# Optimization experiments

Measured on AMD Instinct MI355X. Metric: run time of the kernel, lower is better.

## Reference

```python
import jax, jax.numpy as jnp
import numpy as np


def setup_inputs() -> dict:
    N, E, F, M, D = 50000, 200000, 64, 64, 128
    L = 3
    LAMBS = jnp.array([1.0, 0.1, 0.01], jnp.float32) * 12.0  # lambs * output
    R = int(np.ceil(np.sqrt(N)))  # n_virtuals = 224
    RAW = M * L + F  # raw_message_dimension = 256
    key = jax.random.key(0)
    ks = jax.random.split(key, 16)

    def lin(k, i, o):
        return jax.random.normal(k, (i, o), jnp.float32) / np.float32(np.sqrt(i))

    return dict(
        source_nodes=jax.random.randint(ks[0], (E,), 0, N),
        target_nodes=jax.random.randint(ks[1], (E,), 0, N),
        timestamps=jax.random.uniform(ks[2], (E,), jnp.float32),
        now_time=jnp.ones((1,), jnp.float32),
        predict_IND=0,
        node_features=0.1 * jax.random.normal(ks[3], (N, F), jnp.float32),
        memory=jnp.concatenate([0.05 * jax.random.normal(ks[4], (N, L, M), jnp.float32), jnp.ones((N, L, 1), jnp.float32)], axis=-1),
        last_update=jnp.zeros((N,), jnp.float32),
        virtual_memory=0.05 * jax.random.normal(ks[5], (R, L, M), jnp.float32),
        virtual_last_update=jnp.zeros((R,), jnp.float32),
        A_r=jnp.ones((N, R), jnp.float32) + jax.random.uniform(ks[6], (N, R), jnp.float32) / 10.0,
        static_emb=0.1 * jax.random.normal(ks[7], (N, D), jnp.float32),
        lamb=jnp.array([0.5], jnp.float32),
        lambs=LAMBS,
        mf_W1=lin(ks[8], RAW, RAW // 2), mf_b1=jnp.zeros((RAW // 2,), jnp.float32),
        mf_W2=lin(ks[9], RAW // 2, M), mf_b2=jnp.zeros((M,), jnp.float32),
        ffr_W1=lin(ks[10], RAW, RAW), ffr_b1=jnp.zeros((RAW,), jnp.float32),
        ffr_W2=lin(ks[11], RAW, M), ffr_b2=jnp.zeros((M,), jnp.float32),
        et_W=lin(ks[12], L * M, M), et_b=jnp.zeros((M,), jnp.float32),
        st_W=lin(ks[13], 2 * M, D), st_b=jnp.zeros((D,), jnp.float32),
    )


def reference(source_nodes, target_nodes, timestamps, now_time, predict_IND,
              node_features, memory, last_update, virtual_memory, virtual_last_update,
              A_r, static_emb, lamb, lambs,
              mf_W1, mf_b1, mf_W2, mf_b2, ffr_W1, ffr_b1, ffr_W2, ffr_b2,
              et_W, et_b, st_W, st_b):
    N, L, Mp1 = memory.shape
    M = Mp1 - 1
    R = virtual_memory.shape[0]
    E = source_nodes.shape[0]
    eps = 1e-6

    # exp_lambs embedding of targets: memory ratio [E, L*M]
    mem_t = memory[target_nodes]
    tgt_emb = (mem_t[:, :, :-1] / mem_t[:, :, -1:]).reshape(E, L * M)
    # raw message = [target_embedding, node_features[target], 1]  -> [E, RAW+1]
    src_msg = jnp.concatenate([tgt_emb, node_features[target_nodes], jnp.ones((E, 1), tgt_emb.dtype)], axis=1)

    # exp_lambs aggregation: decay every event to the latest timestamp of its source node
    t_max = jax.ops.segment_max(timestamps, source_nodes, num_segments=N)
    cnt = jax.ops.segment_sum(jnp.ones((E,), timestamps.dtype), source_nodes, num_segments=N)
    has_msg = cnt > 0
    t_max = jnp.where(has_msg, t_max, 0.0)
    w = jnp.exp(-lambs[None, :] * (t_max[source_nodes][:, None] - timestamps[:, None]))  # [E, L]
    agg = jax.ops.segment_sum(w[:, :, None] * src_msg[:, None, :], source_nodes, num_segments=N)  # [N, L, RAW+1]

    # MLP message function on feature channels, carry the weight-count channel along
    feat = agg[:, :, :-1]  # [N, L, RAW]
    h = jax.nn.relu(feat @ mf_W1 + mf_b1)
    msg_feat = jax.nn.relu(h @ mf_W2 + mf_b2)  # [N, L, M]
    messages = jnp.concatenate([msg_feat, agg[:, :, -1:]], axis=-1)  # [N, L, M+1]

    # virtual-node routing: A = softmax(A_r, axis=0) restricted to active nodes
    A = jax.nn.softmax(A_r, axis=0) * has_msg[:, None].astype(A_r.dtype)  # [N, R]
    B = jnp.where(has_msg[:, None, None], feat / jnp.maximum(agg[:, :, -1:], eps), 0.0)  # [N, L, RAW]
    vmid = jnp.einsum('nr,nlf->rlf', A, B)  # [R, L, RAW]
    vh = jax.nn.leaky_relu(vmid @ ffr_W1 + ffr_b1)
    vmsg = jax.nn.leaky_relu(vh @ ffr_W2 + ffr_b2)  # [R, L, M]

    # node memory exp-decay update (only active nodes)
    dt = jnp.where(has_msg, t_max - last_update, 0.0)
    decay = jnp.exp(-lambs[None, :, None] * dt[:, None, None])  # [N, L, 1]
    new_mem = jnp.where(has_msg[:, None, None], memory * decay + messages, memory)
    node_emb = (new_mem[:, :, :-1] / jnp.maximum(new_mem[:, :, -1:], eps)).reshape(N, L * M)

    # virtual memory exp-decay update to now_time
    vdt = now_time[0] - virtual_last_update  # [R]
    vdecay = jnp.exp(-lambs[None, :] * vdt[:, None])  # [R, L]
    new_vmem = virtual_memory * vdecay[:, :, None] + vmsg
    v_emb = new_vmem.reshape(R, L * M)

    r2n = jax.nn.softmax(A_r, axis=1)  # [N, R]
    vnode_emb = r2n @ v_emb  # [N, L*M]

    dyn = jnp.concatenate([node_emb, vnode_emb], axis=0)  # [2N, L*M]
    hh = jax.nn.leaky_relu(dyn @ et_W + et_b)  # [2N, M]
    hh = hh.reshape(2, N, M).transpose(1, 0, 2).reshape(N, 2 * M)
    spat = jax.nn.leaky_relu(hh @ st_W + st_b)  # [N, D]
    return lamb[0] * static_emb + (1.0 - lamb[0]) * spat
```

## Files before the change

kernel.cpp:

```cpp
#include <hip/hip_runtime.h>

static __device__ __forceinline__ float lky(float x) { return x > 0.f ? x : 0.01f * x; }

static __device__ __forceinline__ unsigned short f2bf(float x) {
    unsigned int u = __float_as_uint(x);
    unsigned int r = (u + 0x7FFFu + ((u >> 16) & 1u)) >> 16;
    return (unsigned short)r;
}
static __device__ __forceinline__ float bf2f(unsigned short x) {
    return __uint_as_float((unsigned int)x << 16);
}
static __device__ __forceinline__ unsigned int pack2bf(float lo, float hi) {
    return (unsigned int)f2bf(lo) | ((unsigned int)f2bf(hi) << 16);
}

typedef __attribute__((ext_vector_type(8))) short short8;
typedef __attribute__((ext_vector_type(4))) float f32x4;

constexpr int SN  = 50048;
constexpr int KLV = 608;
constexpr int VCM = 83;
constexpr int NSCAN = 53248;
constexpr int NWG_V = 12 * VCM;
constexpr int NQ_V  = NWG_V / 8;
constexpr int NR_V  = NWG_V % 8;
constexpr int AGG_BLOCKS = 2048;
constexpr int AGG_WAVES  = AGG_BLOCKS * 4;
constexpr int SETUP_BLOCKS = 2048;
constexpr int SETUP_WAVES  = SETUP_BLOCKS * 4;

__global__ __launch_bounds__(256) void k_setup(
        float* t_max, int* cnt, int* cursor, float* colsum,
        const float* __restrict__ mf_W1, unsigned short* __restrict__ W1T,
        const float* __restrict__ mf_W2, unsigned short* __restrict__ W2T,
        const float* __restrict__ et_W,  unsigned short* __restrict__ etWT,
        const float* __restrict__ st_W,  unsigned short* __restrict__ stWT,
        const float* __restrict__ memory, const float* __restrict__ nodef,
        unsigned int* __restrict__ temb, int N, int NP) {
    int gid = blockIdx.x * 256 + threadIdx.x;
    if (gid < N) { t_max[gid] = -1.0f; cursor[gid] = 0; }
    if (gid < NP) cnt[gid] = 0;
    if (gid < 224) colsum[gid] = 0.0f;
    if (gid < 128 * 256) {
        int c = gid / 256, k = gid % 256;
        W1T[gid] = f2bf(mf_W1[k * 128 + c]);
    } else if (gid < 128 * 256 + 64 * 128) {
        int i = gid - 128 * 256;
        int c = i / 128, k = i % 128;
        W2T[i] = f2bf(mf_W2[k * 64 + c]);
    } else if (gid < 128 * 256 + 64 * 128 + 64 * 192) {
        int i = gid - (128 * 256 + 64 * 128);
        int c = i / 192, k = i % 192;
        etWT[i] = f2bf(et_W[k * 64 + c]);
    } else if (gid < 128 * 256 + 64 * 128 + 64 * 192 + 128 * 128) {
        int i = gid - (128 * 256 + 64 * 128 + 64 * 192);
        int c = i / 128, k = i % 128;
        stWT[i] = f2bf(st_W[k * 128 + c]);
    }
    int gw = blockIdx.x * 4 + (threadIdx.x >> 6);
    int lane = threadIdx.x & 63;
    for (int n = gw; n < N; n += SETUP_WAVES) {
        const float* mrow = memory + (size_t)n * 195;
        float d0 = mrow[64], d1 = mrow[129], d2 = mrow[194];
        int f = 2 * lane;
        float den = (f < 64) ? d0 : d1;
        int offA = (f < 64) ? f : f + 1;
        float va0 = mrow[offA] / den;
        float va1 = mrow[offA + 1] / den;
        float vb0, vb1;
        if (lane < 32) {
            vb0 = mrow[130 + 2 * lane] / d2;
            vb1 = mrow[131 + 2 * lane] / d2;
        } else {
            const float* nf = nodef + (size_t)n * 64 + 2 * (lane - 32);
            vb0 = nf[0]; vb1 = nf[1];
        }
        temb[(size_t)n * 128 + lane]      = pack2bf(va0, va1);
        temb[(size_t)n * 128 + 64 + lane] = pack2bf(vb0, vb1);
    }
}

__global__ void k_tmax_cnt(const int* __restrict__ src, const float* __restrict__ ts,
                           float* t_max, int* cnt, int E) {
    int e = blockIdx.x * 256 + threadIdx.x;
    if (e >= E) return;
    int s = src[e];
    atomicMax((int*)(t_max + s), __float_as_int(ts[e]));
    atomicAdd(cnt + s, 1);
}

__global__ __launch_bounds__(1024) void k_scan(const int* __restrict__ cnt,
                                               int* __restrict__ offsets, int N) {
    __shared__ int wsum[16];
    __shared__ int s_run;
    int t = threadIdx.x;
    int lane = t & 63, wid = t >> 6;
    if (t == 0) s_run = 0;
    __syncthreads();
    int nchunk = (N + 4095) >> 12;
    for (int c = 0; c < nchunk; ++c) {
        int i0 = (c << 12) + t * 4;
        int4 v = *(const int4*)(cnt + i0);
        int s = v.x + v.y + v.z + v.w;
        int x = s;
        #pragma unroll
        for (int d = 1; d < 64; d <<= 1) {
            int y = __shfl_up(x, d, 64);
            if (lane >= d) x += y;
        }
        if (lane == 63) wsum[wid] = x;
        __syncthreads();
        int wbase = 0;
        #pragma unroll
        for (int w = 0; w < 16; ++w) wbase += (w < wid) ? wsum[w] : 0;
        int run = s_run;
        int base = run + wbase + x - s;
        if (i0 + 3 < N) {
            int4 o;
            o.x = base; o.y = base + v.x; o.z = o.y + v.y; o.w = o.z + v.z;
            *(int4*)(offsets + i0) = o;
        } else {
            int o = base;
            if (i0 < N) offsets[i0] = o;
            o += v.x;
            if (i0 + 1 < N) offsets[i0 + 1] = o;
            o += v.y;
            if (i0 + 2 < N) offsets[i0 + 2] = o;
            o += v.z;
            if (i0 + 3 < N) offsets[i0 + 3] = o;
        }
        __syncthreads();
        if (t == 1023) s_run = run + wbase + x;
        __syncthreads();
    }
    if (t == 0) offsets[N] = s_run;
}

__global__ void k_scatter(const int* __restrict__ src, const int* __restrict__ tgt,
                          const float* __restrict__ ts, const int* __restrict__ offsets,
                          int* cursor, int2* __restrict__ edat, int E) {
    int e = blockIdx.x * 256 + threadIdx.x;
    if (e >= E) return;
    int s = src[e];
    int pos = offsets[s] + atomicAdd(cursor + s, 1);
    edat[pos] = make_int2(tgt[e], __float_as_int(ts[e]));
}

__global__ __launch_bounds__(256) void k_aexp(
        const float* __restrict__ A_r,
        float* __restrict__ rowsum, float* __restrict__ colsum,
        unsigned short* __restrict__ AexpT, unsigned short* __restrict__ Aexp_rm, int N) {
    __shared__ unsigned short sE[64][228];
    int t = threadIdx.x;
    int n0 = blockIdx.x * 64;
    int maxq = min(64, N - n0) * 56;
    const float4* src = (const float4*)(A_r + (size_t)n0 * 224);
    #pragma unroll
    for (int k = 0; k < 14; ++k) {
        int i = t + k * 256;
        float4 v = (i < maxq) ? src[i] : (float4){-1e30f, -1e30f, -1e30f, -1e30f};
        int row = i / 56, cq = i % 56;
        uint2 pk;
        pk.x = pack2bf(__expf(v.x), __expf(v.y));
        pk.y = pack2bf(__expf(v.z), __expf(v.w));
        *(uint2*)&sE[row][cq * 4] = pk;
    }
    __syncthreads();
    {
        int row = t >> 2, q = t & 3;
        const uint2* p = (const uint2*)&sE[row][q * 56];
        float s = 0.f;
        #pragma unroll
        for (int c = 0; c < 7; ++c) {
            uint2 u = p[c];
            s += __uint_as_float(u.x << 16) + __uint_as_float(u.x & 0xffff0000u)
               + __uint_as_float(u.y << 16) + __uint_as_float(u.y & 0xffff0000u);
        }
        s += __shfl_xor(s, 1, 64);
        s += __shfl_xor(s, 2, 64);
        if (q == 0 && n0 + row < N) rowsum[n0 + row] = s;
    }
    if (t < 224) {
        float s = 0.f;
        #pragma unroll 8
        for (int r = 0; r < 64; ++r) s += bf2f(sE[r][t]);
        atomicAdd(colsum + t, s);
    }
    {
        unsigned int* dst = (unsigned int*)Aexp_rm;
        for (int i = t; i < 64 * 112; i += 256) {
            int n = i / 112, cp = i % 112;
            dst[(size_t)(n0 + n) * 112 + cp] = *(const unsigned int*)&sE[n][2 * cp];
        }
    }
    {
        unsigned int* dst = (unsigned int*)AexpT;
        for (int u = t; u < 224 * 32; u += 256) {
            int r = u >> 5, np = u & 31;
            unsigned int lo = sE[2 * np][r];
            unsigned int hi = sE[2 * np + 1][r];
            dst[(size_t)r * (SN / 2) + (n0 >> 1) + np] = lo | (hi << 16);
        }
    }
}

__global__ __launch_bounds__(256) void k_agg(
        const int2* __restrict__ edat, const int* __restrict__ offsets,
        const float* __restrict__ t_max, const unsigned int* __restrict__ temb,
        const float* __restrict__ lambs,
        unsigned int* __restrict__ aggb, float* __restrict__ cnt3,
        int* __restrict__ has_msg, int N) {
    int gw = blockIdx.x * 4 + (threadIdx.x >> 6);
    int lane = threadIdx.x & 63;
    float lb0 = lambs[0], lb1 = lambs[1], lb2 = lambs[2];
    for (int n = gw; n < SN; n += AGG_WAVES) {
        size_t rb = (size_t)n * 3;
        if (n >= N) {
            #pragma unroll
            for (int l = 0; l < 3; ++l) {
                unsigned int* row = aggb + (rb + l) * 128;
                row[lane] = 0; row[64 + lane] = 0;
                if (lane == 0) cnt3[rb + l] = 0.f;
            }
            continue;
        }
        int beg = offsets[n], end = offsets[n + 1];
        float tm = t_max[n];
        float aa0[3], aa1[3], ab0[3], ab1[3], accc[3];
        #pragma unroll
        for (int l = 0; l < 3; ++l) { aa0[l] = aa1[l] = ab0[l] = ab1[l] = accc[l] = 0.f; }
        for (int idx = beg; idx < end; ++idx) {
            int2 ed = edat[idx];
            int tt = ed.x;
            float d = tm - __int_as_float(ed.y);
            unsigned int ua = temb[(size_t)tt * 128 + lane];
            unsigned int ub = temb[(size_t)tt * 128 + 64 + lane];
            float a0 = __uint_as_float(ua << 16);
            float a1 = __uint_as_float(ua & 0xffff0000u);
            float b0 = __uint_as_float(ub << 16);
            float b1 = __uint_as_float(ub & 0xffff0000u);
            float w0 = __expf(-lb0 * d), w1 = __expf(-lb1 * d), w2 = __expf(-lb2 * d);
            aa0[0] += w0 * a0; aa1[0] += w0 * a1; ab0[0] += w0 * b0; ab1[0] += w0 * b1; accc[0] += w0;
            aa0[1] += w1 * a0; aa1[1] += w1 * a1; ab0[1] += w1 * b0; ab1[1] += w1 * b1; accc[1] += w1;
            aa0[2] += w2 * a0; aa1[2] += w2 * a1; ab0[2] += w2 * b0; ab1[2] += w2 * b1; accc[2] += w2;
        }
        #pragma unroll
        for (int l = 0; l < 3; ++l) {
            unsigned int* row = aggb + (rb + l) * 128;
            row[lane]      = pack2bf(aa0[l], aa1[l]);
            row[64 + lane] = pack2bf(ab0[l], ab1[l]);
            if (lane == 0) cnt3[rb + l] = accc[l];
        }
        if (lane == 0) has_msg[n] = (end > beg) ? 1 : 0;
    }
}

__global__ __launch_bounds__(512, 3) void k_mf_mfma(
        const unsigned short* __restrict__ aggb,
        const unsigned short* __restrict__ W1T, const float* __restrict__ b1,
        const unsigned short* __restrict__ W2T, const float* __restrict__ b2,
        unsigned short* __restrict__ msg_feat, int NROWS) {
    __shared__ unsigned short As[64 * 264];
    __shared__ unsigned short Hs[64 * 136];
    int t = threadIdx.x, lane = t & 63, w = t >> 6;
    int lr = lane & 15, kg = lane >> 4;
    int row0 = blockIdx.x * 64;
    {
        int r = t >> 3, s8 = t & 7;
        const uint4* src = (const uint4*)(aggb + (size_t)(row0 + r) * 256 + s8 * 32);
        uint4* dst = (uint4*)(As + r * 264 + s8 * 32);
        #pragma unroll
        for (int u = 0; u < 4; ++u) dst[u] = src[u];
    }
    __syncthreads();
    int n0 = w * 16;
    f32x4 acc[4];
    #pragma unroll
    for (int m = 0; m < 4; ++m) acc[m] = (f32x4){0.f, 0.f, 0.f, 0.f};
    short8 bfc = *(const short8*)(W1T + (size_t)(n0 + lr) * 256 + kg * 8);
    #pragma unroll
    for (int kk = 0; kk < 8; ++kk) {
        short8 bfn;
        if (kk < 7)
            bfn = *(const short8*)(W1T + (size_t)(n0 + lr) * 256 + (kk + 1) * 32 + kg * 8);
        #pragma unroll
        for (int m = 0; m < 4; ++m) {
            short8 af = *(const short8*)(As + (m * 16 + lr) * 264 + kk * 32 + kg * 8);
            acc[m] = __builtin_amdgcn_mfma_f32_16x16x32_bf16(af, bfc, acc[m], 0, 0, 0);
        }
        bfc = bfn;
    }
    float bb0 = b1[n0 + lr];
    #pragma unroll
    for (int m = 0; m < 4; ++m)
        #pragma unroll
        for (int j = 0; j < 4; ++j) {
            int row = m * 16 + kg * 4 + j;
            Hs[row * 136 + n0 + lr] = f2bf(fmaxf(acc[m][j] + bb0, 0.f));
        }
    __syncthreads();
    int rh = (w >> 2) * 32;
    int c0 = (w & 3) * 16;
    f32x4 a2[2];
    a2[0] = (f32x4){0.f, 0.f, 0.f, 0.f};
    a2[1] = (f32x4){0.f, 0.f, 0.f, 0.f};
    short8 b2c = *(const short8*)(W2T + (size_t)(c0 + lr) * 128 + kg * 8);
    #pragma unroll
    for (int kk = 0; kk < 4; ++kk) {
        short8 b2n;
        if (kk < 3)
            b2n = *(const short8*)(W2T + (size_t)(c0 + lr) * 128 + (kk + 1) * 32 + kg * 8);
        #pragma unroll
        for (int m = 0; m < 2; ++m) {
            short8 af = *(const short8*)(Hs + (rh + m * 16 + lr) * 136 + kk * 32 + kg * 8);
            a2[m] = __builtin_amdgcn_mfma_f32_16x16x32_bf16(af, b2c, a2[m], 0, 0, 0);
        }
        b2c = b2n;
    }
    float b2v = b2[c0 + lr];
    #pragma unroll
    for (int m = 0; m < 2; ++m)
        #pragma unroll
        for (int j = 0; j < 4; ++j) {
            int row = row0 + rh + m * 16 + kg * 4 + j;
            if (row < NROWS)
                msg_feat[(size_t)row * 64 + c0 + lr] = f2bf(fmaxf(a2[m][j] + b2v, 0.f));
        }
}

__global__ __launch_bounds__(256, 4) void k_vmid_mfma(
        const unsigned short* __restrict__ AexpT, const unsigned short* __restrict__ aggb,
        const float* __restrict__ cnt3, float* __restrict__ vpart) {
    __shared__ unsigned short As[112 * 40];
    __shared__ unsigned int BsT[128 * 20];
    int bx = blockIdx.x;
    int xcd = bx & 7, bidx = bx >> 3;
    int virt = (xcd < NR_V) ? xcd * (NQ_V + 1) + bidx
                            : NR_V * (NQ_V + 1) + (xcd - NR_V) * NQ_V + bidx;
    int chunk = virt / 12, tile = virt % 12;
    int r0 = (tile & 1) * 112;
    int ft = tile >> 1;
    int l = ft >> 1, fo = (ft & 1) * 128;
    int t = threadIdx.x, lane = t & 63, w = t >> 6;
    int lr = lane & 15, kg = lane >> 4;
    int np = t >> 4, sg = t & 15;
    f32x4 acc[7][2];
    #pragma unroll
    for (int q = 0; q < 7; ++q) {
        acc[q][0] = (f32x4){0.f, 0.f, 0.f, 0.f};
        acc[q][1] = (f32x4){0.f, 0.f, 0.f, 0.f};
    }
    int nbeg = chunk * KLV;
    int nsteps = min(KLV, SN - nbeg) >> 5;
    int c0 = w * 32 + lr, c1 = c0 + 16;
    int rb0 = c0 * 20 + (kg ^ ((c0 >> 3) & 3)) * 4;
    int rb1 = c1 * 20 + (kg ^ ((c1 >> 3) & 3)) * 4;
    int swz = np ^ ((sg & 3) << 2);
    for (int s = 0; s < nsteps; ++s) {
        int n0 = nbeg + s * 32;
        if (t < 224) {
            int srow = t >> 1, sseg = t & 1;
            const uint4* ap = (const uint4*)(AexpT + (size_t)(r0 + srow) * SN + n0) + sseg * 2;
            uint4 v0 = ap[0];
            uint4 v1 = ap[1];
            *(uint4*)&As[srow * 40 + sseg * 16]     = v0;
            *(uint4*)&As[srow * 40 + sseg * 16 + 8] = v1;
        }
        {
            int na = n0 + 2 * np;
            size_t ra = ((size_t)na * 3 + l) * 256 + fo + sg * 8;
            uint4 va = *(const uint4*)(aggb + ra);
            uint4 vb = *(const uint4*)(aggb + ra + 768);
            float da = 1.f / fmaxf(cnt3[(size_t)na * 3 + l], 1e-6f);
            float db = 1.f / fmaxf(cnt3[(size_t)na * 3 + l + 3], 1e-6f);
            const unsigned short* pa = (const unsigned short*)&va;
            const unsigned short* pb = (const unsigned short*)&vb;
            unsigned int* dst = BsT + sg * 160 + swz;
            #pragma unroll
            for (int j = 0; j < 8; ++j)
                dst[j * 20] = pack2bf(bf2f(pa[j]) * da, bf2f(pb[j]) * db);
        }
        __syncthreads();
        short8 b0 = *(const short8*)((const unsigned short*)(BsT + rb0));
        short8 b1 = *(const short8*)((const unsigned short*)(BsT + rb1));
        #pragma unroll
        for (int q = 0; q < 7; ++q) {
            short8 af = *(const short8*)&As[(q * 16 + lr) * 40 + kg * 8];
            acc[q][0] = __builtin_amdgcn_mfma_f32_16x16x32_bf16(af, b0, acc[q][0], 0, 0, 0);
            acc[q][1] = __builtin_amdgcn_mfma_f32_16x16x32_bf16(af, b1, acc[q][1], 0, 0, 0);
        }
        __syncthreads();
    }
    float* outp = vpart + (size_t)chunk * 172032;
    #pragma unroll
    for (int q = 0; q < 7; ++q) {
        int row = r0 + q * 16 + kg * 4;
        #pragma unroll
        for (int p = 0; p < 2; ++p) {
            int col = l * 256 + fo + w * 32 + p * 16 + lr;
            #pragma unroll
            for (int j = 0; j < 4; ++j)
                outp[(size_t)(row + j) * 768 + col] = acc[q][p][j];
        }
    }
}

__global__ void k_vred(const float* __restrict__ vpart, const float* __restrict__ colsum,
                       float* __restrict__ vmid) {
    int idx = blockIdx.x * 256 + threadIdx.x;
    if (idx >= 224 * 768) return;
    float s = 0.f;
    for (int c = 0; c < VCM; ++c) s += vpart[(long)c * (224 * 768) + idx];
    vmid[idx] = s / colsum[idx / 768];
}

__global__ __launch_bounds__(256) void k_ffr(
        const float* __restrict__ vmid, const float* __restrict__ W1, const float* __restrict__ b1,
        const float* __restrict__ W2, const float* __restrict__ b2,
        const float* __restrict__ vmem, const float* __restrict__ vlast,
        const float* __restrict__ lambs, const float* __restrict__ now_time,
        unsigned short* __restrict__ vembT) {
    __shared__ float sin_[16][260];
    __shared__ float svh[16][260];
    int row0 = blockIdx.x * 16;
    int t = threadIdx.x;
    #pragma unroll
    for (int k = 0; k < 16; ++k) {
        int idx = t + k * 256;
        int r = idx >> 8, f = idx & 255;
        sin_[r][f] = vmid[(long)(row0 + r) * 256 + f];
    }
    __syncthreads();
    {
        int cg = t & 63, rg = t >> 6;
        int c0 = cg * 4, r0 = rg * 4;
        float acc[4][4];
        #pragma unroll
        for (int i = 0; i < 4; ++i)
            #pragma unroll
            for (int j = 0; j < 4; ++j) acc[i][j] = 0.f;
        for (int f0 = 0; f0 < 256; f0 += 4) {
            float4 a[4];
            #pragma unroll
            for (int i = 0; i < 4; ++i) a[i] = *(const float4*)&sin_[r0 + i][f0];
            #pragma unroll
            for (int ff = 0; ff < 4; ++ff) {
                float4 w = *(const float4*)&W1[(long)(f0 + ff) * 256 + c0];
                #pragma unroll
                for (int i = 0; i < 4; ++i) {
                    float av = (&a[i].x)[ff];
                    acc[i][0] += av * w.x; acc[i][1] += av * w.y;
                    acc[i][2] += av * w.z; acc[i][3] += av * w.w;
                }
            }
        }
        #pragma unroll
        for (int i = 0; i < 4; ++i)
            #pragma unroll
            for (int j = 0; j < 4; ++j)
                svh[r0 + i][c0 + j] = lky(acc[i][j] + b1[c0 + j]);
    }
    __syncthreads();
    {
        int cg = t & 31, rg = t >> 5;
        int c0 = cg * 2, r0 = rg * 2;
        float acc[2][2];
        acc[0][0] = acc[0][1] = acc[1][0] = acc[1][1] = 0.f;
        for (int f0 = 0; f0 < 256; f0 += 4) {
            float4 a[2];
            #pragma unroll
            for (int i = 0; i < 2; ++i) a[i] = *(const float4*)&svh[r0 + i][f0];
            #pragma unroll
            for (int ff = 0; ff < 4; ++ff) {
                float2 w = *(const float2*)&W2[(long)(f0 + ff) * 64 + c0];
                #pragma unroll
                for (int i = 0; i < 2; ++i) {
                    float av = (&a[i].x)[ff];
                    acc[i][0] += av * w.x; acc[i][1] += av * w.y;
                }
            }
        }
        float nowv = now_time[0];
        #pragma unroll
        for (int i = 0; i < 2; ++i) {
            int row = row0 + r0 + i;
            int rr = row / 3, l = row % 3;
            float vd = __expf(-lambs[l] * (nowv - vlast[rr]));
            #pragma unroll
            for (int j = 0; j < 2; ++j) {
                float v = lky(acc[i][j] + b2[c0 + j]);
                int m = c0 + j;
                vembT[(size_t)(l * 64 + m) * 224 + rr] =
                    f2bf(vmem[(long)rr * 192 + l * 64 + m] * vd + v);
            }
        }
    }
}

__global__ void k_newmem(const float* __restrict__ memory,
        const unsigned short* __restrict__ msg_feat,
        const float* __restrict__ cnt3, const float* __restrict__ t_max,
        const float* __restrict__ last_update, const int* __restrict__ has_msg,
        const float* __restrict__ lambs, unsigned short* __restrict__ node_emb, int N) {
    int n = blockIdx.x;
    int j = threadIdx.x;
    int l = j >> 6, m = j & 63;
    int has = has_msg[n];
    float dt = has ? (t_max[n] - last_update[n]) : 0.f;
    float decay = __expf(-lambs[l] * dt);
    long mb = (long)n * 195 + l * 65;
    float num = memory[mb + m];
    float den = memory[mb + 64];
    if (has) {
        num = num * decay + bf2f(msg_feat[(size_t)n * 192 + j]);
        den = den * decay + cnt3[(size_t)n * 3 + l];
    }
    node_emb[(size_t)n * 192 + j] = f2bf(num / fmaxf(den, 1e-6f));
}

__global__ __launch_bounds__(256, 4) void k_vnode_mfma(
        const unsigned short* __restrict__ Aexp_rm, const unsigned short* __restrict__ vembT,
        const float* __restrict__ rowsum, unsigned short* __restrict__ vnode_emb, int N) {
    __shared__ unsigned short As[64 * 232];
    __shared__ float sRS[64];
    int t = threadIdx.x, lane = t & 63, w = t >> 6;
    int lr = lane & 15, kg = lane >> 4;
    int row0 = blockIdx.x * 64;
    {
        int r = t >> 2, sg = t & 3;
        const uint4* src = (const uint4*)(Aexp_rm + (size_t)(row0 + r) * 224 + sg * 56);
        uint4* dst = (uint4*)(As + r * 232 + sg * 56);
        #pragma unroll
        for (int u = 0; u < 7; ++u) dst[u] = src[u];
    }
    if (t < 64) sRS[t] = rowsum[min(row0 + t, N - 1)];
    __syncthreads();
    int n0 = w * 48;
    f32x4 acc[4][3];
    #pragma unroll
    for (int m = 0; m < 4; ++m)
        #pragma unroll
        for (int nt = 0; nt < 3; ++nt) acc[m][nt] = (f32x4){0.f, 0.f, 0.f, 0.f};
    #pragma unroll
    for (int kk = 0; kk < 7; ++kk) {
        short8 bf[3];
        #pragma unroll
        for (int nt = 0; nt < 3; ++nt)
            bf[nt] = *(const short8*)(vembT + (size_t)(n0 + nt * 16 + lr) * 224 + kk * 32 + kg * 8);
        #pragma unroll
        for (int m = 0; m < 4; ++m) {
            short8 af = *(const short8*)(As + (m * 16 + lr) * 232 + kk * 32 + kg * 8);
            #pragma unroll
            for (int nt = 0; nt < 3; ++nt)
                acc[m][nt] = __builtin_amdgcn_mfma_f32_16x16x32_bf16(af, bf[nt], acc[m][nt], 0, 0, 0);
        }
    }
    #pragma unroll
    for (int m = 0; m < 4; ++m)
        #pragma unroll
        for (int j = 0; j < 4; ++j) {
            int row = row0 + m * 16 + kg * 4 + j;
            if (row < N) {
                float inv = 1.f / sRS[row - row0];
                #pragma unroll
                for (int nt = 0; nt < 3; ++nt)
                    vnode_emb[(size_t)row * 192 + n0 + nt * 16 + lr] = f2bf(acc[m][nt][j] * inv);
            }
        }
}

__global__ __launch_bounds__(256, 4) void k_et_st_mfma(
        const unsigned short* __restrict__ ne, const unsigned short* __restrict__ ve,
        const unsigned short* __restrict__ etWT, const float* __restrict__ etb,
        const unsigned short* __restrict__ stWT, const float* __restrict__ stb,
        const float* __restrict__ stat, const float* __restrict__ lamb,
        float* __restrict__ out, int N) {
    __shared__ unsigned short As[64 * 200];
    __shared__ unsigned short Hs[32 * 136];
    int t = threadIdx.x, lane = t & 63, w = t >> 6;
    int lr = lane & 15, kg = lane >> 4;
    int row0 = blockIdx.x * 32;
    {
        int r = t >> 3, s8 = t & 7;
        const uint4* sn = (const uint4*)(ne + (size_t)(row0 + r) * 192 + s8 * 24);
        const uint4* sv = (const uint4*)(ve + (size_t)(row0 + r) * 192 + s8 * 24);
        uint4* dn = (uint4*)(As + (size_t)r * 200 + s8 * 24);
        uint4* dv = (uint4*)(As + (size_t)(32 + r) * 200 + s8 * 24);
        #pragma unroll
        for (int u = 0; u < 3; ++u) { dn[u] = sn[u]; dv[u] = sv[u]; }
    }
    __syncthreads();
    int c0 = w * 16;
    f32x4 acc[2][2];
    #pragma unroll
    for (int h = 0; h < 2; ++h)
        #pragma unroll
        for (int m = 0; m < 2; ++m) acc[h][m] = (f32x4){0.f, 0.f, 0.f, 0.f};
    #pragma unroll
    for (int kk = 0; kk < 6; ++kk) {
        short8 bf = *(const short8*)(etWT + (size_t)(c0 + lr) * 192 + kk * 32 + kg * 8);
        #pragma unroll
        for (int h = 0; h < 2; ++h)
            #pragma unroll
            for (int m = 0; m < 2; ++m) {
                short8 af = *(const short8*)(As + (size_t)(h * 32 + m * 16 + lr) * 200 + kk * 32 + kg * 8);
                acc[h][m] = __builtin_amdgcn_mfma_f32_16x16x32_bf16(af, bf, acc[h][m], 0, 0, 0);
            }
    }
    float bb = etb[c0 + lr];
    #pragma unroll
    for (int h = 0; h < 2; ++h)
        #pragma unroll
        for (int m = 0; m < 2; ++m)
            #pragma unroll
            for (int j = 0; j < 4; ++j)
                Hs[(m * 16 + kg * 4 + j) * 136 + h * 64 + c0 + lr] = f2bf(lky(acc[h][m][j] + bb));
    __syncthreads();
    int c0s = w * 32;
    f32x4 a2[2][2];
    #pragma unroll
    for (int m = 0; m < 2; ++m) { a2[m][0] = (f32x4){0.f,0.f,0.f,0.f}; a2[m][1] = (f32x4){0.f,0.f,0.f,0.f}; }
    #pragma unroll
    for (int kk = 0; kk < 4; ++kk) {
        short8 bf0 = *(const short8*)(stWT + (size_t)(c0s + lr) * 128 + kk * 32 + kg * 8);
        short8 bf1 = *(const short8*)(stWT + (size_t)(c0s + 16 + lr) * 128 + kk * 32 + kg * 8);
        #pragma unroll
        for (int m = 0; m < 2; ++m) {
            short8 af = *(const short8*)(Hs + (m * 16 + lr) * 136 + kk * 32 + kg * 8);
            a2[m][0] = __builtin_amdgcn_mfma_f32_16x16x32_bf16(af, bf0, a2[m][0], 0, 0, 0);
            a2[m][1] = __builtin_amdgcn_mfma_f32_16x16x32_bf16(af, bf1, a2[m][1], 0, 0, 0);
        }
    }
    float lam = lamb[0];
    float sb0 = stb[c0s + lr], sb1 = stb[c0s + 16 + lr];
    #pragma unroll
    for (int m = 0; m < 2; ++m)
        #pragma unroll
        for (int j = 0; j < 4; ++j) {
            int n = row0 + m * 16 + kg * 4 + j;
            if (n < N) {
                int ca = c0s + lr, cb = c0s + 16 + lr;
                float va = lky(a2[m][0][j] + sb0);
                float vb = lky(a2[m][1][j] + sb1);
                out[(size_t)n * 128 + ca] = lam * stat[(size_t)n * 128 + ca] + (1.f - lam) * va;
                out[(size_t)n * 128 + cb] = lam * stat[(size_t)n * 128 + cb] + (1.f - lam) * vb;
            }
        }
}

extern "C" void kernel_launch(void* const* d_in, const int* in_sizes, int n_in,
                              void* d_out, int out_size, void* d_ws, size_t ws_size,
                              hipStream_t stream) {
    const int*   src        = (const int*)d_in[0];
    const int*   tgt        = (const int*)d_in[1];
    const float* ts         = (const float*)d_in[2];
    const float* now_time   = (const float*)d_in[3];
    const float* nodef      = (const float*)d_in[5];
    const float* memory     = (const float*)d_in[6];
    const float* last_upd   = (const float*)d_in[7];
    const float* vmem       = (const float*)d_in[8];
    const float* vlast      = (const float*)d_in[9];
    const float* A_r        = (const float*)d_in[10];
    const float* static_emb = (const float*)d_in[11];
    const float* lamb       = (const float*)d_in[12];
    const float* lambs      = (const float*)d_in[13];
    const float* mf_W1      = (const float*)d_in[14];
    const float* mf_b1      = (const float*)d_in[15];
    const float* mf_W2      = (const float*)d_in[16];
    const float* mf_b2      = (const float*)d_in[17];
    const float* ffr_W1     = (const float*)d_in[18];
    const float* ffr_b1     = (const float*)d_in[19];
    const float* ffr_W2     = (const float*)d_in[20];
    const float* ffr_b2     = (const float*)d_in[21];
    const float* et_W       = (const float*)d_in[22];
    const float* et_b       = (const float*)d_in[23];
    const float* st_W       = (const float*)d_in[24];
    const float* st_b       = (const float*)d_in[25];

    int E = in_sizes[0];
    int N = in_sizes[7];

    float* ws = (float*)d_ws;
    size_t off = 0;
    auto alloc = [&](size_t nf) { float* p = ws + off; off += (nf + 63) & ~(size_t)63; return p; };
    unsigned short* aggb  = (unsigned short*)alloc((size_t)SN * 384);
    unsigned short* msg_feat = (unsigned short*)alloc((size_t)N * 96);
    unsigned short* AexpT   = (unsigned short*)alloc((size_t)224 * SN / 2);
    unsigned short* Aexp_rm = (unsigned short*)alloc((size_t)SN * 224 / 2);
    float* tv_union = alloc((size_t)VCM * 172032);
    float* vmid     = alloc(224 * 768);
    unsigned short* vembT = (unsigned short*)alloc((size_t)192 * 224 / 2 + 64);
    float* t_max    = alloc(N);
    float* rowsum   = alloc(N);
    float* cnt3     = alloc((size_t)SN * 3);
    float* colsum   = alloc(256);
    unsigned short* W1T  = (unsigned short*)alloc(128 * 256 / 2);
    unsigned short* W2T  = (unsigned short*)alloc(64 * 128 / 2);
    unsigned short* etWT = (unsigned short*)alloc(64 * 192 / 2);
    unsigned short* stWT = (unsigned short*)alloc(128 * 128 / 2);
    int*   cnt      = (int*)alloc(NSCAN);
    int*   offsets  = (int*)alloc(N + 1);
    int*   cursor   = (int*)alloc(N);
    int2*  edat     = (int2*)alloc((size_t)E * 2);
    int*   has_msg  = (int*)alloc(N);
    if (off * sizeof(float) > ws_size) return;

    unsigned int* temb = (unsigned int*)tv_union;
    float* vpart = tv_union;
    unsigned short* node_emb  = (unsigned short*)aggb;
    unsigned short* vnode_emb = node_emb + (size_t)N * 192;

    k_setup<<<SETUP_BLOCKS, 256, 0, stream>>>(t_max, cnt, cursor, colsum,
                                              mf_W1, W1T, mf_W2, W2T, et_W, etWT, st_W, stWT,
                                              memory, nodef, temb, N, NSCAN);
    k_tmax_cnt<<<(E + 255) / 256, 256, 0, stream>>>(src, ts, t_max, cnt, E);
    k_scan<<<1, 1024, 0, stream>>>(cnt, offsets, N);
    k_scatter<<<(E + 255) / 256, 256, 0, stream>>>(src, tgt, ts, offsets, cursor, edat, E);
    k_aexp<<<SN / 64, 256, 0, stream>>>(A_r, rowsum, colsum, AexpT, Aexp_rm, N);
    k_agg<<<AGG_BLOCKS, 256, 0, stream>>>(edat, offsets, t_max, temb,
                                          lambs, (unsigned int*)aggb, cnt3, has_msg, N);
    k_mf_mfma<<<SN * 3 / 64, 512, 0, stream>>>(aggb, W1T, mf_b1, W2T, mf_b2, msg_feat, N * 3);
    k_vmid_mfma<<<NWG_V, 256, 0, stream>>>(AexpT, aggb, cnt3, vpart);
    k_vred<<<(224 * 768 + 255) / 256, 256, 0, stream>>>(vpart, colsum, vmid);
    k_ffr<<<42, 256, 0, stream>>>(vmid, ffr_W1, ffr_b1, ffr_W2, ffr_b2, vmem, vlast,
                                  lambs, now_time, vembT);
    k_newmem<<<N, 192, 0, stream>>>(memory, msg_feat, cnt3, t_max, last_upd, has_msg,
                                    lambs, node_emb, N);
    k_vnode_mfma<<<SN / 64, 256, 0, stream>>>(Aexp_rm, vembT, rowsum, vnode_emb, N);
    k_et_st_mfma<<<SN / 32, 256, 0, stream>>>(node_emb, vnode_emb, etWT, et_b, stWT, st_b,
                                              static_emb, lamb, (float*)d_out, N);
}
```

Measured before the change: 346.9 us.

## Fuse message-MLP and virtual-mid kernels into one interleaved launch

Merges the per-row message MLP kernel and the virtual-node mid aggregation kernel into a single launch with 512-thread blocks. Block IDs are spread so vmid tiles are interleaved evenly among MLP tiles, letting both independent workloads share the GPU concurrently instead of running back to back. The aim is to remove a launch boundary and fill idle CUs during each kernel's tail. The vmid path now runs in 512-thread blocks with half the threads idle, and shared memory is sized for the larger of the two, which may lower occupancy.

```diff
diff --git a/kernel.cpp b/kernel.cpp
--- a/kernel.cpp
+++ b/kernel.cpp
@@ -24,6 +24,8 @@
 constexpr int NWG_V = 12 * VCM;
 constexpr int NQ_V  = NWG_V / 8;
 constexpr int NR_V  = NWG_V % 8;
+constexpr int MF_WG = SN * 3 / 64;
+constexpr int TOT_WG = NWG_V + MF_WG;
 constexpr int AGG_BLOCKS = 2048;
 constexpr int AGG_WAVES  = AGG_BLOCKS * 4;
 constexpr int SETUP_BLOCKS = 2048;
@@ -255,153 +257,161 @@
     }
 }
 
-__global__ __launch_bounds__(512, 3) void k_mf_mfma(
+__global__ __launch_bounds__(512, 3) void k_mf_vmid(
         const unsigned short* __restrict__ aggb,
         const unsigned short* __restrict__ W1T, const float* __restrict__ b1,
         const unsigned short* __restrict__ W2T, const float* __restrict__ b2,
-        unsigned short* __restrict__ msg_feat, int NROWS) {
-    __shared__ unsigned short As[64 * 264];
-    __shared__ unsigned short Hs[64 * 136];
-    int t = threadIdx.x, lane = t & 63, w = t >> 6;
+        unsigned short* __restrict__ msg_feat, int NROWS,
+        const unsigned short* __restrict__ AexpT, const float* __restrict__ cnt3,
+        float* __restrict__ vpart) {
+    __shared__ __align__(16) char smem[51200];
+    int bid = blockIdx.x;
+    int t = threadIdx.x, lane = t & 63;
     int lr = lane & 15, kg = lane >> 4;
-    int row0 = blockIdx.x * 64;
-    {
-        int r = t >> 3, s8 = t & 7;
-        const uint4* src = (const uint4*)(aggb + (size_t)(row0 + r) * 256 + s8 * 32);
-        uint4* dst = (uint4*)(As + r * 264 + s8 * 32);
-        #pragma unroll
-        for (int u = 0; u < 4; ++u) dst[u] = src[u];
-    }
-    __syncthreads();
-    int n0 = w * 16;
-    f32x4 acc[4];
-    #pragma unroll
-    for (int m = 0; m < 4; ++m) acc[m] = (f32x4){0.f, 0.f, 0.f, 0.f};
-    short8 bfc = *(const short8*)(W1T + (size_t)(n0 + lr) * 256 + kg * 8);
-    #pragma unroll
-    for (int kk = 0; kk < 8; ++kk) {
-        short8 bfn;
-        if (kk < 7)
-            bfn = *(const short8*)(W1T + (size_t)(n0 + lr) * 256 + (kk + 1) * 32 + kg * 8);
-        #pragma unroll
-        for (int m = 0; m < 4; ++m) {
-            short8 af = *(const short8*)(As + (m * 16 + lr) * 264 + kk * 32 + kg * 8);
-            acc[m] = __builtin_amdgcn_mfma_f32_16x16x32_bf16(af, bfc, acc[m], 0, 0, 0);
-        }
-        bfc = bfn;
-    }
-    float bb0 = b1[n0 + lr];
-    #pragma unroll
-    for (int m = 0; m < 4; ++m)
-        #pragma unroll
-        for (int j = 0; j < 4; ++j) {
-            int row = m * 16 + kg * 4 + j;
-            Hs[row * 136 + n0 + lr] = f2bf(fmaxf(acc[m][j] + bb0, 0.f));
-        }
-    __syncthreads();
-    int rh = (w >> 2) * 32;
-    int c0 = (w & 3) * 16;
-    f32x4 a2[2];
-    a2[0] = (f32x4){0.f, 0.f, 0.f, 0.f};
-    a2[1] = (f32x4){0.f, 0.f, 0.f, 0.f};
-    short8 b2c = *(const short8*)(W2T + (size_t)(c0 + lr) * 128 + kg * 8);
-    #pragma unroll
-    for (int kk = 0; kk < 4; ++kk) {
-        short8 b2n;
-        if (kk < 3)
-            b2n = *(const short8*)(W2T + (size_t)(c0 + lr) * 128 + (kk + 1) * 32 + kg * 8);
-        #pragma unroll
-        for (int m = 0; m < 2; ++m) {
-            short8 af = *(const short8*)(Hs + (rh + m * 16 + lr) * 136 + kk * 32 + kg * 8);
-            a2[m] = __builtin_amdgcn_mfma_f32_16x16x32_bf16(af, b2c, a2[m], 0, 0, 0);
-        }
-        b2c = b2n;
-    }
-    float b2v = b2[c0 + lr];
-    #pragma unroll
-    for (int m = 0; m < 2; ++m)
-        #pragma unroll
-        for (int j = 0; j < 4; ++j) {
-            int row = row0 + rh + m * 16 + kg * 4 + j;
-            if (row < NROWS)
-                msg_feat[(size_t)row * 64 + c0 + lr] = f2bf(fmaxf(a2[m][j] + b2v, 0.f));
-        }
-}
-
-__global__ __launch_bounds__(256, 4) void k_vmid_mfma(
-        const unsigned short* __restrict__ AexpT, const unsigned short* __restrict__ aggb,
-        const float* __restrict__ cnt3, float* __restrict__ vpart) {
-    __shared__ unsigned short As[112 * 40];
-    __shared__ unsigned int BsT[128 * 20];
-    int bx = blockIdx.x;
-    int xcd = bx & 7, bidx = bx >> 3;
-    int virt = (xcd < NR_V) ? xcd * (NQ_V + 1) + bidx
-                            : NR_V * (NQ_V + 1) + (xcd - NR_V) * NQ_V + bidx;
-    int chunk = virt / 12, tile = virt % 12;
-    int r0 = (tile & 1) * 112;
-    int ft = tile >> 1;
-    int l = ft >> 1, fo = (ft & 1) * 128;
-    int t = threadIdx.x, lane = t & 63, w = t >> 6;
-    int lr = lane & 15, kg = lane >> 4;
-    int np = t >> 4, sg = t & 15;
-    f32x4 acc[7][2];
-    #pragma unroll
-    for (int q = 0; q < 7; ++q) {
-        acc[q][0] = (f32x4){0.f, 0.f, 0.f, 0.f};
-        acc[q][1] = (f32x4){0.f, 0.f, 0.f, 0.f};
-    }
-    int nbeg = chunk * KLV;
-    int nsteps = min(KLV, SN - nbeg) >> 5;
-    int c0 = w * 32 + lr, c1 = c0 + 16;
-    int rb0 = c0 * 20 + (kg ^ ((c0 >> 3) & 3)) * 4;
-    int rb1 = c1 * 20 + (kg ^ ((c1 >> 3) & 3)) * 4;
-    int swz = np ^ ((sg & 3) << 2);
-    for (int s = 0; s < nsteps; ++s) {
-        int n0 = nbeg + s * 32;
-        if (t < 224) {
-            int srow = t >> 1, sseg = t & 1;
-            const uint4* ap = (const uint4*)(AexpT + (size_t)(r0 + srow) * SN + n0) + sseg * 2;
-            uint4 v0 = ap[0];
-            uint4 v1 = ap[1];
-            *(uint4*)&As[srow * 40 + sseg * 16]     = v0;
-            *(uint4*)&As[srow * 40 + sseg * 16 + 8] = v1;
-        }
+    int q0 = (int)(((long)bid * NWG_V) / TOT_WG);
+    int q1 = (int)(((long)(bid + 1) * NWG_V) / TOT_WG);
+    if (q1 > q0) {
+        unsigned short* As = (unsigned short*)smem;
+        unsigned int*  BsT = (unsigned int*)(smem + 8960);
+        int bx = q0;
+        int xcd = bx & 7, bidx = bx >> 3;
+        int virt = (xcd < NR_V) ? xcd * (NQ_V + 1) + bidx
+                                : NR_V * (NQ_V + 1) + (xcd - NR_V) * NQ_V + bidx;
+        int chunk = virt / 12, tile = virt % 12;
+        int r0 = (tile & 1) * 112;
+        int ft = tile >> 1;
+        int l = ft >> 1, fo = (ft & 1) * 128;
+        int w4 = t >> 6;
+        int np = t >> 4, sg = t & 15;
+        f32x4 acc[7][2];
+        #pragma unroll
+        for (int q = 0; q < 7; ++q) {
+            acc[q][0] = (f32x4){0.f, 0.f, 0.f, 0.f};
+            acc[q][1] = (f32x4){0.f, 0.f, 0.f, 0.f};
+        }
+        int nbeg = chunk * KLV;
+        int nsteps = min(KLV, SN - nbeg) >> 5;
+        int c0 = (w4 & 3) * 32 + lr, c1 = c0 + 16;
+        int rb0 = c0 * 20 + (kg ^ ((c0 >> 3) & 3)) * 4;
+        int rb1 = c1 * 20 + (kg ^ ((c1 >> 3) & 3)) * 4;
+        int swz = (np & 15) ^ ((sg & 3) << 2);
+        for (int s = 0; s < nsteps; ++s) {
+            int n0 = nbeg + s * 32;
+            if (t < 224) {
+                int srow = t >> 1, sseg = t & 1;
+                const uint4* ap = (const uint4*)(AexpT + (size_t)(r0 + srow) * SN + n0) + sseg * 2;
+                uint4 v0 = ap[0];
+                uint4 v1 = ap[1];
+                *(uint4*)&As[srow * 40 + sseg * 16]     = v0;
+                *(uint4*)&As[srow * 40 + sseg * 16 + 8] = v1;
+            }
+            if (t < 256) {
+                int na = n0 + 2 * np;
+                size_t ra = ((size_t)na * 3 + l) * 256 + fo + sg * 8;
+                uint4 va = *(const uint4*)(aggb + ra);
+                uint4 vb = *(const uint4*)(aggb + ra + 768);
+                float da = 1.f / fmaxf(cnt3[(size_t)na * 3 + l], 1e-6f);
+                float db = 1.f / fmaxf(cnt3[(size_t)na * 3 + l + 3], 1e-6f);
+                const unsigned short* pa = (const unsigned short*)&va;
+                const unsigned short* pb = (const unsigned short*)&vb;
+                unsigned int* dst = BsT + sg * 160 + swz;
+                #pragma unroll
+                for (int j = 0; j < 8; ++j)
+                    dst[j * 20] = pack2bf(bf2f(pa[j]) * da, bf2f(pb[j]) * db);
+            }
+            __syncthreads();
+            if (t < 256) {
+                short8 b0v = *(const short8*)((const unsigned short*)(BsT + rb0));
+                short8 b1v = *(const short8*)((const unsigned short*)(BsT + rb1));
+                #pragma unroll
+                for (int q = 0; q < 7; ++q) {
+                    short8 af = *(const short8*)&As[(q * 16 + lr) * 40 + kg * 8];
+                    acc[q][0] = __builtin_amdgcn_mfma_f32_16x16x32_bf16(af, b0v, acc[q][0], 0, 0, 0);
+                    acc[q][1] = __builtin_amdgcn_mfma_f32_16x16x32_bf16(af, b1v, acc[q][1], 0, 0, 0);
+                }
+            }
+            __syncthreads();
+        }
+        if (t < 256) {
+            float* outp = vpart + (size_t)chunk * 172032;
+            #pragma unroll
+            for (int q = 0; q < 7; ++q) {
+                int row = r0 + q * 16 + kg * 4;
+                #pragma unroll
+                for (int p = 0; p < 2; ++p) {
+                    int col = l * 256 + fo + (w4 & 3) * 32 + p * 16 + lr;
+                    #pragma unroll
+                    for (int j = 0; j < 4; ++j)
+                        outp[(size_t)(row + j) * 768 + col] = acc[q][p][j];
+                }
+            }
+        }
+    } else {
+        unsigned short* As = (unsigned short*)smem;
+        unsigned short* Hs = (unsigned short*)(smem + 33792);
+        int w = t >> 6;
+        int row0 = (bid - q0) * 64;
         {
-            int na = n0 + 2 * np;
-            size_t ra = ((size_t)na * 3 + l) * 256 + fo + sg * 8;
-            uint4 va = *(const uint4*)(aggb + ra);
-            uint4 vb = *(const uint4*)(aggb + ra + 768);
-            float da = 1.f / fmaxf(cnt3[(size_t)na * 3 + l], 1e-6f);
-            float db = 1.f / fmaxf(cnt3[(size_t)na * 3 + l + 3], 1e-6f);
-            const unsigned short* pa = (const unsigned short*)&va;
-            const unsigned short* pb = (const unsigned short*)&vb;
-            unsigned int* dst = BsT + sg * 160 + swz;
-            #pragma unroll
-            for (int j = 0; j < 8; ++j)
-                dst[j * 20] = pack2bf(bf2f(pa[j]) * da, bf2f(pb[j]) * db);
+            int r = t >> 3, s8 = t & 7;
+            const uint4* src = (const uint4*)(aggb + (size_t)(row0 + r) * 256 + s8 * 32);
+            uint4* dst = (uint4*)(As + r * 264 + s8 * 32);
+            #pragma unroll
+            for (int u = 0; u < 4; ++u) dst[u] = src[u];
         }
         __syncthreads();
-        short8 b0 = *(const short8*)((const unsigned short*)(BsT + rb0));
-        short8 b1 = *(const short8*)((const unsigned short*)(BsT + rb1));
-        #pragma unroll
-        for (int q = 0; q < 7; ++q) {
-            short8 af = *(const short8*)&As[(q * 16 + lr) * 40 + kg * 8];
-            acc[q][0] = __builtin_amdgcn_mfma_f32_16x16x32_bf16(af, b0, acc[q][0], 0, 0, 0);
-            acc[q][1] = __builtin_amdgcn_mfma_f32_16x16x32_bf16(af, b1, acc[q][1], 0, 0, 0);
-        }
+        int n0 = w * 16;
+        f32x4 acc[4];
+        #pragma unroll
+        for (int m = 0; m < 4; ++m) acc[m] = (f32x4){0.f, 0.f, 0.f, 0.f};
+        short8 bfc = *(const short8*)(W1T + (size_t)(n0 + lr) * 256 + kg * 8);
+        #pragma unroll
+        for (int kk = 0; kk < 8; ++kk) {
+            short8 bfn;
+            if (kk < 7)
+                bfn = *(const short8*)(W1T + (size_t)(n0 + lr) * 256 + (kk + 1) * 32 + kg * 8);
+            #pragma unroll
+            for (int m = 0; m < 4; ++m) {
+                short8 af = *(const short8*)(As + (m * 16 + lr) * 264 + kk * 32 + kg * 8);
+                acc[m] = __builtin_amdgcn_mfma_f32_16x16x32_bf16(af, bfc, acc[m], 0, 0, 0);
+            }
+            bfc = bfn;
+        }
+        float bb0 = b1[n0 + lr];
+        #pragma unroll
+        for (int m = 0; m < 4; ++m)
+            #pragma unroll
+            for (int j = 0; j < 4; ++j) {
+                int row = m * 16 + kg * 4 + j;
+                Hs[row * 136 + n0 + lr] = f2bf(fmaxf(acc[m][j] + bb0, 0.f));
+            }
         __syncthreads();
-    }
-    float* outp = vpart + (size_t)chunk * 172032;
-    #pragma unroll
-    for (int q = 0; q < 7; ++q) {
-        int row = r0 + q * 16 + kg * 4;
-        #pragma unroll
-        for (int p = 0; p < 2; ++p) {
-            int col = l * 256 + fo + w * 32 + p * 16 + lr;
-            #pragma unroll
-            for (int j = 0; j < 4; ++j)
-                outp[(size_t)(row + j) * 768 + col] = acc[q][p][j];
-        }
+        int rh = (w >> 2) * 32;
+        int c0 = (w & 3) * 16;
+        f32x4 a2[2];
+        a2[0] = (f32x4){0.f, 0.f, 0.f, 0.f};
+        a2[1] = (f32x4){0.f, 0.f, 0.f, 0.f};
+        short8 b2c = *(const short8*)(W2T + (size_t)(c0 + lr) * 128 + kg * 8);
+        #pragma unroll
+        for (int kk = 0; kk < 4; ++kk) {
+            short8 b2n;
+            if (kk < 3)
+                b2n = *(const short8*)(W2T + (size_t)(c0 + lr) * 128 + (kk + 1) * 32 + kg * 8);
+            #pragma unroll
+            for (int m = 0; m < 2; ++m) {
+                short8 af = *(const short8*)(Hs + (rh + m * 16 + lr) * 136 + kk * 32 + kg * 8);
+                a2[m] = __builtin_amdgcn_mfma_f32_16x16x32_bf16(af, b2c, a2[m], 0, 0, 0);
+            }
+            b2c = b2n;
+        }
+        float b2v = b2[c0 + lr];
+        #pragma unroll
+        for (int m = 0; m < 2; ++m)
+            #pragma unroll
+            for (int j = 0; j < 4; ++j) {
+                int row = row0 + rh + m * 16 + kg * 4 + j;
+                if (row < NROWS)
+                    msg_feat[(size_t)row * 64 + c0 + lr] = f2bf(fmaxf(a2[m][j] + b2v, 0.f));
+            }
     }
 }
 
@@ -719,8 +729,8 @@
     k_aexp<<<SN / 64, 256, 0, stream>>>(A_r, rowsum, colsum, AexpT, Aexp_rm, N);
     k_agg<<<AGG_BLOCKS, 256, 0, stream>>>(edat, offsets, t_max, temb,
                                           lambs, (unsigned int*)aggb, cnt3, has_msg, N);
-    k_mf_mfma<<<SN * 3 / 64, 512, 0, stream>>>(aggb, W1T, mf_b1, W2T, mf_b2, msg_feat, N * 3);
-    k_vmid_mfma<<<NWG_V, 256, 0, stream>>>(AexpT, aggb, cnt3, vpart);
+    k_mf_vmid<<<TOT_WG, 512, 0, stream>>>(aggb, W1T, mf_b1, W2T, mf_b2, msg_feat, N * 3,
+                                          AexpT, cnt3, vpart);
     k_vred<<<(224 * 768 + 255) / 256, 256, 0, stream>>>(vpart, colsum, vmid);
     k_ffr<<<42, 256, 0, stream>>>(vmid, ffr_W1, ffr_b1, ffr_W2, ffr_b2, vmem, vlast,
                                   lambs, now_time, vembT);
```

After: 369.0 us. +6.4%, slower.
